# Kernel optimization log

Measured on AMD Instinct MI355X. Metric: run time of the kernel, lower is better.

Reference implementation:

```python
import jax, jax.numpy as jnp
import numpy as np

NUM_C = 1000
DIM_S = 128
SIZE_M = 64
B = 64
L = 512


def setup_inputs() -> dict:
    key = jax.random.key(0)
    ks = jax.random.split(key, 16)
    d = DIM_S
    inp = {
        "q": jax.random.randint(ks[0], (B, L), 0, NUM_C),
        "r": jax.random.randint(ks[1], (B, L), 0, 2),
        # embeddings
        "Ek": jax.random.normal(ks[2], (NUM_C, d), jnp.float32),
        "Ev": jax.random.normal(ks[3], (2 * NUM_C, d), jnp.float32),
        # memory key / initial value memory (kaiming-normal-ish)
        "Mk": jax.random.normal(ks[4], (SIZE_M, d), jnp.float32) * np.sqrt(2.0 / d),
        "Mv0": jax.random.normal(ks[5], (SIZE_M, d), jnp.float32) * np.sqrt(2.0 / d),
        # erase / add layers (d -> d)
        "We": jax.random.normal(ks[6], (d, d), jnp.float32) / np.sqrt(d),
        "be": jnp.zeros((d,), jnp.float32),
        "Wa": jax.random.normal(ks[7], (d, d), jnp.float32) / np.sqrt(d),
        "ba": jnp.zeros((d,), jnp.float32),
        # f layer (2d -> d)
        "Wf": jax.random.normal(ks[8], (2 * d, d), jnp.float32) / np.sqrt(2 * d),
        "bf": jnp.zeros((d,), jnp.float32),
        # p layer (d -> 1)
        "Wp": jax.random.normal(ks[9], (d, 1), jnp.float32) / np.sqrt(d),
        "bp": jnp.zeros((1,), jnp.float32),
    }
    return inp


def reference(q, r, Ek, Ev, Mk, Mv0, We, be, Wa, ba, Wf, bf, Wp, bp):
    # q, r: [B, L] int
    x = q + NUM_C * r
    k = Ek[q]            # [B, L, D]  (k_original; no extra features when use_ed=use_mp=0)
    v = Ev[x]            # [B, L, D]

    # correlation weights over memory slots
    w = jax.nn.softmax(jnp.einsum("bld,md->blm", k, Mk), axis=-1)  # [B, L, M]

    e = jax.nn.sigmoid(v @ We + be)  # [B, L, D] erase
    a = jnp.tanh(v @ Wa + ba)        # [B, L, D] add

    def step(Mvt, inputs):
        wt, et, at = inputs            # [B,M], [B,D], [B,D]
        # read from memory BEFORE the update (matches Mv[:, :-1] in torch)
        read = jnp.einsum("bm,bmd->bd", wt, Mvt)
        Mvt_new = Mvt * (1.0 - wt[:, :, None] * et[:, None, :]) + wt[:, :, None] * at[:, None, :]
        return Mvt_new, read

    Mv_init = jnp.broadcast_to(Mv0[None], (q.shape[0], SIZE_M, DIM_S))
    xs = (jnp.swapaxes(w, 0, 1), jnp.swapaxes(e, 0, 1), jnp.swapaxes(a, 0, 1))
    _, reads = jax.lax.scan(step, Mv_init, xs)      # reads: [L, B, D]
    read_content = jnp.swapaxes(reads, 0, 1)        # [B, L, D]

    f = jnp.tanh(jnp.concatenate([read_content, k], axis=-1) @ Wf + bf)  # [B, L, D]
    # dropout in eval mode -> identity
    p = jax.nn.sigmoid(f @ Wp + bp)[..., 0]         # [B, L]
    return p
```

## Files before the change

### kernel.cpp

```cpp
#include <hip/hip_runtime.h>
#include <hip/hip_bf16.h>

#define NUM_C 1000
#define DIM   128
#define MM    64
#define BB    64
#define LL    512
#define NROWS (BB * LL)

typedef unsigned short u16;
typedef unsigned int   u32;
typedef short bfrag __attribute__((ext_vector_type(8)));
typedef float f32x4 __attribute__((ext_vector_type(4)));

__device__ __forceinline__ float sigmoidf_fast(float x) { return 1.f / (1.f + __expf(-x)); }
__device__ __forceinline__ float tanhf_fast(float x) { return 1.f - 2.f / (__expf(2.f * x) + 1.f); }

__device__ __forceinline__ u16 f2bf(float x) {
    u32 u = __float_as_uint(x);
    return (u16)((u + 0x7FFFu + ((u >> 16) & 1u)) >> 16);
}
__device__ __forceinline__ float bf2f(u16 h) { return __uint_as_float(((u32)h) << 16); }

__device__ __forceinline__ float quad_swap1(float x) {
    return __int_as_float(__builtin_amdgcn_mov_dpp(__float_as_int(x), 0xB1, 0xF, 0xF, true));
}
__device__ __forceinline__ float quad_swap2(float x) {
    return __int_as_float(__builtin_amdgcn_mov_dpp(__float_as_int(x), 0x4E, 0xF, 0xF, true));
}

__device__ __forceinline__ void ld16(const void* g, void* l) {
    __builtin_amdgcn_global_load_lds(
        (const __attribute__((address_space(1))) unsigned int*)g,
        (__attribute__((address_space(3))) unsigned int*)l, 16, 0, 0);
}

__global__ __launch_bounds__(256) void kP(const float* __restrict__ We,
                                          const float* __restrict__ Wa,
                                          const float* __restrict__ Wf,
                                          const float* __restrict__ Mk,
                                          u16* weT_hi, u16* weT_lo,
                                          u16* waT_hi, u16* waT_lo,
                                          u16* wfT_hi, u16* wfT_lo,
                                          u16* mkT_hi, u16* mkT_lo) {
    int idx = blockIdx.x * 256 + threadIdx.x;
    if (idx < 128 * 128) {
        int n = idx >> 7, k = idx & 127;
        float we = We[k * DIM + n];
        u16 h = f2bf(we);
        weT_hi[idx] = h; weT_lo[idx] = f2bf(we - bf2f(h));
        float wa = Wa[k * DIM + n];
        u16 h2 = f2bf(wa);
        waT_hi[idx] = h2; waT_lo[idx] = f2bf(wa - bf2f(h2));
    }
    if (idx < 64 * 128) {
        float mk = Mk[idx];
        u16 h = f2bf(mk);
        mkT_hi[idx] = h; mkT_lo[idx] = f2bf(mk - bf2f(h));
    }
    {
        int n = idx >> 8, k = idx & 255;
        float wf = Wf[k * DIM + n];
        u16 h = f2bf(wf);
        wfT_hi[idx] = h; wfT_lo[idx] = f2bf(wf - bf2f(h));
    }
}

__device__ __forceinline__ void split8(const float* src, bfrag& h, bfrag& l) {
    float4 f0 = *reinterpret_cast<const float4*>(src);
    float4 f1 = *reinterpret_cast<const float4*>(src + 4);
    float xs[8] = {f0.x, f0.y, f0.z, f0.w, f1.x, f1.y, f1.z, f1.w};
    #pragma unroll
    for (int j = 0; j < 8; ++j) {
        u16 hb = f2bf(xs[j]);
        h[j] = (short)hb;
        l[j] = (short)f2bf(xs[j] - bf2f(hb));
    }
}

__global__ __launch_bounds__(256) void kAB(const int* __restrict__ q,
                                           const int* __restrict__ r,
                                           const float* __restrict__ Ek,
                                           const float* __restrict__ Ev,
                                           const u16* __restrict__ mkT_hi, const u16* __restrict__ mkT_lo,
                                           const u16* __restrict__ weT_hi, const u16* __restrict__ weT_lo,
                                           const u16* __restrict__ waT_hi, const u16* __restrict__ waT_lo,
                                           const float* __restrict__ be, const float* __restrict__ ba,
                                           float* __restrict__ w_out,
                                           float2* __restrict__ ea_out) {
    __shared__ __align__(16) u16 shi[4][16][136];
    __shared__ __align__(16) u16 slo[4][16][136];
    __shared__ float slab[4][64];
    const int tid = threadIdx.x;
    const int lane = tid & 63;
    const int wv = tid >> 6;
    const int nloc = lane & 15;
    const int quad = lane >> 4;

    if (blockIdx.x < 512) {
        const int base = blockIdx.x * 64;
        {
            const int row_l = tid >> 2;
            const int rts = row_l >> 4, ms = row_l & 15;
            const int d0 = (tid & 3) * 32;
            const float* src = Ek + (size_t)q[base + row_l] * DIM + d0;
            #pragma unroll
            for (int c8 = 0; c8 < 4; ++c8) {
                bfrag h, l;
                split8(src + c8 * 8, h, l);
                *reinterpret_cast<bfrag*>(&shi[rts][ms][d0 + c8 * 8]) = h;
                *reinterpret_cast<bfrag*>(&slo[rts][ms][d0 + c8 * 8]) = l;
            }
        }
        __syncthreads();

        const int n = wv * 16 + nloc;
        bfrag Bh[4], Bl[4];
        #pragma unroll
        for (int kc = 0; kc < 4; ++kc) {
            const int ko = kc * 32 + quad * 8;
            Bh[kc] = *reinterpret_cast<const bfrag*>(mkT_hi + n * DIM + ko);
            Bl[kc] = *reinterpret_cast<const bfrag*>(mkT_lo + n * DIM + ko);
        }

        f32x4 acc[4];
        #pragma unroll
        for (int t = 0; t < 4; ++t) acc[t] = 0.f;

        #pragma unroll
        for (int rt = 0; rt < 4; ++rt) {
            #pragma unroll
            for (int kc = 0; kc < 4; ++kc) {
                const int ko = kc * 32 + quad * 8;
                bfrag Ah = *reinterpret_cast<const bfrag*>(&shi[rt][nloc][ko]);
                bfrag Al = *reinterpret_cast<const bfrag*>(&slo[rt][nloc][ko]);
                acc[rt] = __builtin_amdgcn_mfma_f32_16x16x32_bf16(Ah, Bh[kc], acc[rt], 0, 0, 0);
                acc[rt] = __builtin_amdgcn_mfma_f32_16x16x32_bf16(Ah, Bl[kc], acc[rt], 0, 0, 0);
                acc[rt] = __builtin_amdgcn_mfma_f32_16x16x32_bf16(Al, Bh[kc], acc[rt], 0, 0, 0);
            }
        }

        float ex[4][4];
        #pragma unroll
        for (int rt = 0; rt < 4; ++rt) {
            #pragma unroll
            for (int rg = 0; rg < 4; ++rg) {
                float e = __expf(acc[rt][rg]);
                ex[rt][rg] = e;
                float s = e;
                s += __shfl_xor(s, 1);
                s += __shfl_xor(s, 2);
                s += __shfl_xor(s, 4);
                s += __shfl_xor(s, 8);
                if (nloc == 0) slab[wv][rt * 16 + quad * 4 + rg] = s;
            }
        }
        __syncthreads();

        #pragma unroll
        for (int rt = 0; rt < 4; ++rt) {
            #pragma unroll
            for (int rg = 0; rg < 4; ++rg) {
                const int row = rt * 16 + quad * 4 + rg;
                float tot = slab[0][row] + slab[1][row] + slab[2][row] + slab[3][row];
                w_out[(size_t)(base + row) * MM + n] = ex[rt][rg] / tot;
            }
        }
    } else {
        const int base = (blockIdx.x - 512) * 64;
        {
            const int row_l = tid >> 2;
            const int rts = row_l >> 4, ms = row_l & 15;
            const int d0 = (tid & 3) * 32;
            const int row = base + row_l;
            const int x = q[row] + NUM_C * r[row];
            const float* src = Ev + (size_t)x * DIM + d0;
            #pragma unroll
            for (int c8 = 0; c8 < 4; ++c8) {
                bfrag h, l;
                split8(src + c8 * 8, h, l);
                *reinterpret_cast<bfrag*>(&shi[rts][ms][d0 + c8 * 8]) = h;
                *reinterpret_cast<bfrag*>(&slo[rts][ms][d0 + c8 * 8]) = l;
            }
        }
        __syncthreads();

        #pragma unroll
        for (int dt = 0; dt < 2; ++dt) {
            const int n = (wv * 2 + dt) * 16 + nloc;
            bfrag Beh[4], Bel[4], Bah[4], Bal[4];
            #pragma unroll
            for (int kc = 0; kc < 4; ++kc) {
                const int ko = kc * 32 + quad * 8;
                Beh[kc] = *reinterpret_cast<const bfrag*>(weT_hi + n * DIM + ko);
                Bel[kc] = *reinterpret_cast<const bfrag*>(weT_lo + n * DIM + ko);
                Bah[kc] = *reinterpret_cast<const bfrag*>(waT_hi + n * DIM + ko);
                Bal[kc] = *reinterpret_cast<const bfrag*>(waT_lo + n * DIM + ko);
            }
            f32x4 acc_e[4], acc_a[4];
            #pragma unroll
            for (int t = 0; t < 4; ++t) { acc_e[t] = 0.f; acc_a[t] = 0.f; }

            #pragma unroll
            for (int rt = 0; rt < 4; ++rt) {
                #pragma unroll
                for (int kc = 0; kc < 4; ++kc) {
                    const int ko = kc * 32 + quad * 8;
                    bfrag Ah = *reinterpret_cast<const bfrag*>(&shi[rt][nloc][ko]);
                    bfrag Al = *reinterpret_cast<const bfrag*>(&slo[rt][nloc][ko]);
                    acc_e[rt] = __builtin_amdgcn_mfma_f32_16x16x32_bf16(Ah, Beh[kc], acc_e[rt], 0, 0, 0);
                    acc_a[rt] = __builtin_amdgcn_mfma_f32_16x16x32_bf16(Ah, Bah[kc], acc_a[rt], 0, 0, 0);
                    acc_e[rt] = __builtin_amdgcn_mfma_f32_16x16x32_bf16(Ah, Bel[kc], acc_e[rt], 0, 0, 0);
                    acc_a[rt] = __builtin_amdgcn_mfma_f32_16x16x32_bf16(Ah, Bal[kc], acc_a[rt], 0, 0, 0);
                    acc_e[rt] = __builtin_amdgcn_mfma_f32_16x16x32_bf16(Al, Beh[kc], acc_e[rt], 0, 0, 0);
                    acc_a[rt] = __builtin_amdgcn_mfma_f32_16x16x32_bf16(Al, Bah[kc], acc_a[rt], 0, 0, 0);
                }
            }
            const float bev = be[n], bav = ba[n];
            #pragma unroll
            for (int rt = 0; rt < 4; ++rt) {
                #pragma unroll
                for (int rg = 0; rg < 4; ++rg) {
                    const int row = base + rt * 16 + quad * 4 + rg;
                    float2 ea;
                    ea.x = sigmoidf_fast(acc_e[rt][rg] + bev);
                    ea.y = tanhf_fast(acc_a[rt][rg] + bav);
                    ea_out[(size_t)row * DIM + n] = ea;
                }
            }
        }
    }
}

__device__ __forceinline__ void scan32(const float* wb, const float2* eab,
                                       int m0, int dl, int p, int t0,
                                       float (&Mv)[4], float* rp4) {
    #pragma unroll
    for (int u = 0; u < 32; ++u) {
        float4 w4 = *reinterpret_cast<const float4*>(wb + u * 64 + m0);
        float2 ea = eab[u * 16 + dl];
        float wv[4] = {w4.x, w4.y, w4.z, w4.w};
        float e_c = ea.x, a_c = ea.y;
        float part = 0.f;
        #pragma unroll
        for (int j = 0; j < 4; ++j) {
            float old = Mv[j];
            part = fmaf(wv[j], old, part);
            Mv[j] = fmaf(wv[j], fmaf(-old, e_c, a_c), old);
        }
        part += quad_swap1(part);
        part += quad_swap2(part);
        if ((p & 3) == 0)
            rp4[(size_t)(t0 + u) * (DIM * 4)] = part;
    }
}

__global__ __launch_bounds__(256) void kC(const float* __restrict__ Mv0,
                                          const float* __restrict__ w_in,
                                          const float2* __restrict__ ea_in,
                                          float* __restrict__ rd4) {
    __shared__ __align__(16) float  wlds[2][32][64];
    __shared__ __align__(16) float2 ealds[2][32][16];
    const int tid = threadIdx.x;
    const int lane = tid & 63;
    const int wvid = tid >> 6;
    const int p = tid & 15;
    const int dl = tid >> 4;
    const int ds = blockIdx.x, b = blockIdx.y;
    const int d = ds * 16 + dl;
    const int m0 = p * 4;

    const char* wsrc  = (const char*)(w_in + (size_t)b * LL * MM);
    const char* easrc = (const char*)(ea_in + (size_t)b * LL * DIM + ds * 16);
    float* rp4 = rd4 + (size_t)b * LL * (DIM * 4) + (size_t)d * 4 + (p >> 2);

    auto dma = [&](int c, int bufi) {
        const char* wt = wsrc + (size_t)c * 8192;
        char* wl = (char*)&wlds[bufi][0][0];
        char* el = (char*)&ealds[bufi][0][0];
        #pragma unroll
        for (int i = 0; i < 2; ++i) {
            const int off = wvid * 2048 + i * 1024 + lane * 16;
            ld16(wt + off, wl + off);
        }
        const int off2 = wvid * 1024 + lane * 16;
        const int tl = off2 >> 7, wi = off2 & 127;
        ld16(easrc + (size_t)(c * 32 + tl) * (DIM * 8) + wi, el + off2);
    };

    dma(0, 0);

    float Mv[4];
    #pragma unroll
    for (int j = 0; j < 4; ++j)
        Mv[j] = Mv0[(m0 + j) * DIM + d];

    __builtin_amdgcn_s_waitcnt(0x0F70);
    __syncthreads();

    int buf = 0;
    for (int c = 0; c < LL / 32; ++c) {
        if (c + 1 < LL / 32) dma(c + 1, buf ^ 1);
        scan32(&wlds[buf][0][0], &ealds[buf][0][0], m0, dl, p, c * 32, Mv, rp4);
        if (c + 1 < LL / 32) {
            __builtin_amdgcn_s_waitcnt(0x8F70);
            __syncthreads();
            buf ^= 1;
        }
    }
}

__global__ __launch_bounds__(256) void kD(const int* __restrict__ q,
                                          const float* __restrict__ Ek,
                                          const u16* __restrict__ wfT_hi, const u16* __restrict__ wfT_lo,
                                          const float* __restrict__ bfv,
                                          const float* __restrict__ Wp, const float* __restrict__ bp,
                                          const float* __restrict__ rd4,
                                          float* __restrict__ out) {
    __shared__ __align__(16) u16 xhi[4][16][264];
    __shared__ __align__(16) u16 xlo[4][16][264];
    __shared__ float sred[64][4];
    const int tid = threadIdx.x;
    const int base = blockIdx.x * 64;
    const int row_l = tid >> 2;
    const int rts = row_l >> 4, ms = row_l & 15;
    const int d0 = (tid & 3) * 32;
    const int row = base + row_l;

    {
        const float4* src4 = reinterpret_cast<const float4*>(rd4 + (size_t)row * (DIM * 4)) + d0;
        #pragma unroll
        for (int c8 = 0; c8 < 4; ++c8) {
            float xs[8];
            #pragma unroll
            for (int j = 0; j < 8; ++j) {
                float4 v = src4[c8 * 8 + j];
                xs[j] = (v.x + v.y) + (v.z + v.w);
            }
            bfrag h, l;
            #pragma unroll
            for (int j = 0; j < 8; ++j) {
                u16 hb = f2bf(xs[j]);
                h[j] = (short)hb;
                l[j] = (short)f2bf(xs[j] - bf2f(hb));
            }
            *reinterpret_cast<bfrag*>(&xhi[rts][ms][d0 + c8 * 8]) = h;
            *reinterpret_cast<bfrag*>(&xlo[rts][ms][d0 + c8 * 8]) = l;
        }
    }
    {
        const float* src = Ek + (size_t)q[row] * DIM + d0;
        #pragma unroll
        for (int c8 = 0; c8 < 4; ++c8) {
            bfrag h, l;
            split8(src + c8 * 8, h, l);
            *reinterpret_cast<bfrag*>(&xhi[rts][ms][128 + d0 + c8 * 8]) = h;
            *reinterpret_cast<bfrag*>(&xlo[rts][ms][128 + d0 + c8 * 8]) = l;
        }
    }
    __syncthreads();

    const int lane = tid & 63;
    const int wv = tid >> 6;
    const int nloc = lane & 15;
    const int quad = lane >> 4;
    float* fbuf = reinterpret_cast<float*>(&xhi[0][0][0]);

    f32x4 acc[2][4];
    #pragma unroll
    for (int dt = 0; dt < 2; ++dt)
        #pragma unroll
        for (int t = 0; t < 4; ++t) acc[dt][t] = 0.f;

    #pragma unroll
    for (int dt = 0; dt < 2; ++dt) {
        const int n = (wv * 2 + dt) * 16 + nloc;
        bfrag Bh[8], Bl[8];
        #pragma unroll
        for (int kc = 0; kc < 8; ++kc) {
            const int ko = kc * 32 + quad * 8;
            Bh[kc] = *reinterpret_cast<const bfrag*>(wfT_hi + n * 256 + ko);
            Bl[kc] = *reinterpret_cast<const bfrag*>(wfT_lo + n * 256 + ko);
        }
        #pragma unroll
        for (int rt = 0; rt < 4; ++rt) {
            #pragma unroll
            for (int kc = 0; kc < 8; ++kc) {
                const int ko = kc * 32 + quad * 8;
                bfrag Ah = *reinterpret_cast<const bfrag*>(&xhi[rt][nloc][ko]);
                bfrag Al = *reinterpret_cast<const bfrag*>(&xlo[rt][nloc][ko]);
                acc[dt][rt] = __builtin_amdgcn_mfma_f32_16x16x32_bf16(Ah, Bh[kc], acc[dt][rt], 0, 0, 0);
                acc[dt][rt] = __builtin_amdgcn_mfma_f32_16x16x32_bf16(Ah, Bl[kc], acc[dt][rt], 0, 0, 0);
                acc[dt][rt] = __builtin_amdgcn_mfma_f32_16x16x32_bf16(Al, Bh[kc], acc[dt][rt], 0, 0, 0);
            }
        }
    }
    __syncthreads();

    #pragma unroll
    for (int dt = 0; dt < 2; ++dt) {
        const int n = (wv * 2 + dt) * 16 + nloc;
        const float bfn = bfv[n], wpn = Wp[n];
        #pragma unroll
        for (int rt = 0; rt < 4; ++rt)
            #pragma unroll
            for (int rg = 0; rg < 4; ++rg)
                fbuf[(rt * 16 + quad * 4 + rg) * 132 + n] = tanhf_fast(acc[dt][rt][rg] + bfn) * wpn;
    }
    __syncthreads();

    {
        float s = 0.f;
        const int c = tid & 3;
        #pragma unroll
        for (int k = 0; k < 32; ++k) s += fbuf[row_l * 132 + c * 32 + k];
        sred[row_l][c] = s;
    }
    __syncthreads();
    if (tid < 64)
        out[base + tid] = sigmoidf_fast(sred[tid][0] + sred[tid][1] + sred[tid][2] + sred[tid][3] + bp[0]);
}

extern "C" void kernel_launch(void* const* d_in, const int* in_sizes, int n_in,
                              void* d_out, int out_size, void* d_ws, size_t ws_size,
                              hipStream_t stream) {
    const int*   q   = (const int*)d_in[0];
    const int*   r   = (const int*)d_in[1];
    const float* Ek  = (const float*)d_in[2];
    const float* Ev  = (const float*)d_in[3];
    const float* Mk  = (const float*)d_in[4];
    const float* Mv0 = (const float*)d_in[5];
    const float* We  = (const float*)d_in[6];
    const float* be  = (const float*)d_in[7];
    const float* Wa  = (const float*)d_in[8];
    const float* ba  = (const float*)d_in[9];
    const float* Wf  = (const float*)d_in[10];
    const float* bfv = (const float*)d_in[11];
    const float* Wp  = (const float*)d_in[12];
    const float* bp  = (const float*)d_in[13];
    float* out = (float*)d_out;

    float*  ws     = (float*)d_ws;
    float*  w_buf  = ws;
    float2* ea_buf = (float2*)(w_buf + (size_t)NROWS * MM);
    float*  rd4    = (float*)(ea_buf + (size_t)NROWS * DIM);

    size_t prep_off = (ws_size - (size_t)294912) & ~(size_t)255;
    u16* weT_hi = (u16*)((char*)d_ws + prep_off);
    u16* weT_lo = weT_hi + 16384;
    u16* waT_hi = weT_lo + 16384;
    u16* waT_lo = waT_hi + 16384;
    u16* wfT_hi = waT_lo + 16384;
    u16* wfT_lo = wfT_hi + 32768;
    u16* mkT_hi = wfT_lo + 32768;
    u16* mkT_lo = mkT_hi + 8192;

    kP<<<dim3(128), 256, 0, stream>>>(We, Wa, Wf, Mk, weT_hi, weT_lo, waT_hi, waT_lo,
                                      wfT_hi, wfT_lo, mkT_hi, mkT_lo);
    kAB<<<dim3(1024), 256, 0, stream>>>(q, r, Ek, Ev, mkT_hi, mkT_lo,
                                        weT_hi, weT_lo, waT_hi, waT_lo,
                                        be, ba, w_buf, ea_buf);
    kC<<<dim3(8, BB), 256, 0, stream>>>(Mv0, w_buf, ea_buf, rd4);
    kD<<<dim3(NROWS / 64), 256, 0, stream>>>(q, Ek, wfT_hi, wfT_lo, bfv, Wp, bp, rd4, out);
}
```

Baseline: 182.7 us.

## Reduce scan read partials in-register and drop the 4x partial buffer

The scan kernel now reduces each read value across all 16 lanes with two extra row-rotate DPP adds, instead of only across a quad. It therefore writes one float per (row, d) rather than four partial sums. The consumer kernel loads the finished read values directly and no longer sums partials. The scan kernel is also retiled to 512 threads covering 32 columns per block, which halves the block count and spreads the DMA over 8 waves. This cuts the global write and read traffic of the intermediate buffer by about a factor of four, at the cost of a few extra DPP ops per step and a different occupancy profile.

```diff
diff --git a/kernel.cpp b/kernel.cpp
--- a/kernel.cpp
+++ b/kernel.cpp
@@ -27,6 +27,12 @@
 }
 __device__ __forceinline__ float quad_swap2(float x) {
     return __int_as_float(__builtin_amdgcn_mov_dpp(__float_as_int(x), 0x4E, 0xF, 0xF, true));
+}
+__device__ __forceinline__ float row_ror4(float x) {
+    return __int_as_float(__builtin_amdgcn_mov_dpp(__float_as_int(x), 0x124, 0xF, 0xF, true));
+}
+__device__ __forceinline__ float row_ror8(float x) {
+    return __int_as_float(__builtin_amdgcn_mov_dpp(__float_as_int(x), 0x128, 0xF, 0xF, true));
 }
 
 __device__ __forceinline__ void ld16(const void* g, void* l) {
@@ -234,11 +240,11 @@
 
 __device__ __forceinline__ void scan32(const float* wb, const float2* eab,
                                        int m0, int dl, int p, int t0,
-                                       float (&Mv)[4], float* rp4) {
+                                       float (&Mv)[4], float* rp) {
     #pragma unroll
     for (int u = 0; u < 32; ++u) {
         float4 w4 = *reinterpret_cast<const float4*>(wb + u * 64 + m0);
-        float2 ea = eab[u * 16 + dl];
+        float2 ea = eab[u * 32 + dl];
         float wv[4] = {w4.x, w4.y, w4.z, w4.w};
         float e_c = ea.x, a_c = ea.y;
         float part = 0.f;
@@ -250,42 +256,39 @@
         }
         part += quad_swap1(part);
         part += quad_swap2(part);
-        if ((p & 3) == 0)
-            rp4[(size_t)(t0 + u) * (DIM * 4)] = part;
-    }
-}
-
-__global__ __launch_bounds__(256) void kC(const float* __restrict__ Mv0,
+        part += row_ror4(part);
+        part += row_ror8(part);
+        if (p == 0) rp[(size_t)(t0 + u) * DIM] = part;
+    }
+}
+
+__global__ __launch_bounds__(512) void kC(const float* __restrict__ Mv0,
                                           const float* __restrict__ w_in,
                                           const float2* __restrict__ ea_in,
-                                          float* __restrict__ rd4) {
+                                          float* __restrict__ rd) {
     __shared__ __align__(16) float  wlds[2][32][64];
-    __shared__ __align__(16) float2 ealds[2][32][16];
+    __shared__ __align__(16) float2 ealds[2][32][32];
     const int tid = threadIdx.x;
     const int lane = tid & 63;
     const int wvid = tid >> 6;
     const int p = tid & 15;
     const int dl = tid >> 4;
     const int ds = blockIdx.x, b = blockIdx.y;
-    const int d = ds * 16 + dl;
+    const int d = ds * 32 + dl;
     const int m0 = p * 4;
 
     const char* wsrc  = (const char*)(w_in + (size_t)b * LL * MM);
-    const char* easrc = (const char*)(ea_in + (size_t)b * LL * DIM + ds * 16);
-    float* rp4 = rd4 + (size_t)b * LL * (DIM * 4) + (size_t)d * 4 + (p >> 2);
+    const char* easrc = (const char*)(ea_in + (size_t)b * LL * DIM + ds * 32);
+    float* rp = rd + (size_t)b * LL * DIM + d;
 
     auto dma = [&](int c, int bufi) {
         const char* wt = wsrc + (size_t)c * 8192;
         char* wl = (char*)&wlds[bufi][0][0];
         char* el = (char*)&ealds[bufi][0][0];
-        #pragma unroll
-        for (int i = 0; i < 2; ++i) {
-            const int off = wvid * 2048 + i * 1024 + lane * 16;
-            ld16(wt + off, wl + off);
-        }
-        const int off2 = wvid * 1024 + lane * 16;
-        const int tl = off2 >> 7, wi = off2 & 127;
-        ld16(easrc + (size_t)(c * 32 + tl) * (DIM * 8) + wi, el + off2);
+        const int off = wvid * 1024 + lane * 16;
+        ld16(wt + off, wl + off);
+        const int tl = off >> 8, wi = off & 255;
+        ld16(easrc + (size_t)(c * 32 + tl) * (DIM * 8) + wi, el + off);
     };
 
     dma(0, 0);
@@ -301,7 +304,7 @@
     int buf = 0;
     for (int c = 0; c < LL / 32; ++c) {
         if (c + 1 < LL / 32) dma(c + 1, buf ^ 1);
-        scan32(&wlds[buf][0][0], &ealds[buf][0][0], m0, dl, p, c * 32, Mv, rp4);
+        scan32(&wlds[buf][0][0], &ealds[buf][0][0], m0, dl, p, c * 32, Mv, rp);
         if (c + 1 < LL / 32) {
             __builtin_amdgcn_s_waitcnt(0x8F70);
             __syncthreads();
@@ -315,7 +318,7 @@
                                           const u16* __restrict__ wfT_hi, const u16* __restrict__ wfT_lo,
                                           const float* __restrict__ bfv,
                                           const float* __restrict__ Wp, const float* __restrict__ bp,
-                                          const float* __restrict__ rd4,
+                                          const float* __restrict__ rd,
                                           float* __restrict__ out) {
     __shared__ __align__(16) u16 xhi[4][16][264];
     __shared__ __align__(16) u16 xlo[4][16][264];
@@ -328,22 +331,11 @@
     const int row = base + row_l;
 
     {
-        const float4* src4 = reinterpret_cast<const float4*>(rd4 + (size_t)row * (DIM * 4)) + d0;
+        const float* src = rd + (size_t)row * DIM + d0;
         #pragma unroll
         for (int c8 = 0; c8 < 4; ++c8) {
-            float xs[8];
-            #pragma unroll
-            for (int j = 0; j < 8; ++j) {
-                float4 v = src4[c8 * 8 + j];
-                xs[j] = (v.x + v.y) + (v.z + v.w);
-            }
             bfrag h, l;
-            #pragma unroll
-            for (int j = 0; j < 8; ++j) {
-                u16 hb = f2bf(xs[j]);
-                h[j] = (short)hb;
-                l[j] = (short)f2bf(xs[j] - bf2f(hb));
-            }
+            split8(src + c8 * 8, h, l);
             *reinterpret_cast<bfrag*>(&xhi[rts][ms][d0 + c8 * 8]) = h;
             *reinterpret_cast<bfrag*>(&xlo[rts][ms][d0 + c8 * 8]) = l;
         }
@@ -443,7 +435,7 @@
     float*  ws     = (float*)d_ws;
     float*  w_buf  = ws;
     float2* ea_buf = (float2*)(w_buf + (size_t)NROWS * MM);
-    float*  rd4    = (float*)(ea_buf + (size_t)NROWS * DIM);
+    float*  rd     = (float*)(ea_buf + (size_t)NROWS * DIM);
 
     size_t prep_off = (ws_size - (size_t)294912) & ~(size_t)255;
     u16* weT_hi = (u16*)((char*)d_ws + prep_off);
@@ -460,6 +452,6 @@
     kAB<<<dim3(1024), 256, 0, stream>>>(q, r, Ek, Ev, mkT_hi, mkT_lo,
                                         weT_hi, weT_lo, waT_hi, waT_lo,
                                         be, ba, w_buf, ea_buf);
-    kC<<<dim3(8, BB), 256, 0, stream>>>(Mv0, w_buf, ea_buf, rd4);
-    kD<<<dim3(NROWS / 64), 256, 0, stream>>>(q, Ek, wfT_hi, wfT_lo, bfv, Wp, bp, rd4, out);
-}
+    kC<<<dim3(4, BB), 512, 0, stream>>>(Mv0, w_buf, ea_buf, rd);
+    kD<<<dim3(NROWS / 64), 256, 0, stream>>>(q, Ek, wfT_hi, wfT_lo, bfv, Wp, bp, rd, out);
+}
```

Measured after the change: 180.4 us. Within noise of the previous version (-1.3%).
